# Kernel tuning notes

Hardware: AMD Instinct MI355X
Metric: run time of the kernel (lower is better)

Reference implementation:

```python
import jax, jax.numpy as jnp
import numpy as np

INP = 64   # inplanes
PLN = 64   # planes
LOC = 64   # loc_planes
EPS = 1e-5


def _linear_init(key, fan_in, fan_out):
    # torch nn.Linear default: U(-1/sqrt(fan_in), 1/sqrt(fan_in)) for W and b
    kw, kb = jax.random.split(key)
    bound = 1.0 / np.sqrt(fan_in)
    W = jax.random.uniform(kw, (fan_in, fan_out), jnp.float32, -bound, bound)
    b = jax.random.uniform(kb, (fan_out,), jnp.float32, -bound, bound)
    return W, b


def setup_inputs() -> dict:
    key = jax.random.key(0)
    ks = jax.random.split(key, 8)
    B, N = 8, 4096
    img_fea = jax.random.normal(ks[0], (B, N, INP), jnp.float32)
    loc_fea = jax.random.normal(ks[1], (B, N, LOC), jnp.float32)
    W11, b11 = _linear_init(ks[2], INP + LOC, INP)
    W12, b12 = _linear_init(ks[3], INP, INP)
    W21, b21 = _linear_init(ks[4], INP + LOC, INP)
    W22, b22 = _linear_init(ks[5], INP, INP * PLN)
    W3, b3 = _linear_init(ks[6], PLN, PLN)
    ln_g = jnp.ones((PLN,), jnp.float32)
    ln_b = jnp.zeros((PLN,), jnp.float32)
    return {
        "img_fea": img_fea, "loc_fea": loc_fea,
        "W11": W11, "b11": b11, "W12": W12, "b12": b12,
        "W21": W21, "b21": b21, "W22": W22, "b22": b22,
        "ln_g": ln_g, "ln_b": ln_b, "W3": W3, "b3": b3,
    }


def reference(img_fea, loc_fea, W11, b11, W12, b12, W21, b21, W22, b22,
              ln_g, ln_b, W3, b3):
    B, N, C = img_fea.shape
    cat_fea = jnp.concatenate([img_fea, loc_fea], axis=2)  # [B,N,INP+LOC]
    # branch 1: per-token input vector
    w11 = jax.nn.relu(cat_fea @ W11 + b11)                 # [B,N,INP]
    w12 = w11 @ W12 + b12                                  # [B,N,INP]
    # branch 2: per-token weight matrix generation
    w21 = jax.nn.relu(cat_fea @ W21 + b21)                 # [B,N,INP]
    w22 = (w21 @ W22 + b22).reshape(B, N, INP, PLN)        # [B,N,INP,PLN]
    # batched tiny matvec: (1,INP) @ (INP,PLN) per token
    x = jnp.einsum('bni,bnio->bno', w12, w22)              # [B,N,PLN]
    # LayerNorm over last dim + ReLU
    mu = jnp.mean(x, axis=-1, keepdims=True)
    var = jnp.mean(jnp.square(x - mu), axis=-1, keepdims=True)
    x = (x - mu) * jax.lax.rsqrt(var + EPS) * ln_g + ln_b
    x = jax.nn.relu(x)
    # final linear (no activation)
    return x @ W3 + b3
```

## Files before the change

kernel.cpp:

```cpp
#include <hip/hip_runtime.h>
#include <cstdint>


typedef __bf16 bf16x4 __attribute__((ext_vector_type(4)));
typedef __bf16 bf16x8 __attribute__((ext_vector_type(8)));
typedef float  f32x4  __attribute__((ext_vector_type(4)));

#define MFMA16(A, B, C) __builtin_amdgcn_mfma_f32_16x16x32_bf16(A, B, C, 0, 0, 0)

#define OFF_BT22 0
#define OFF_W11  266240
#define OFF_W21  274432
#define OFF_W12  282624
#define OFF_W3   286720

__global__ __launch_bounds__(256) void prep_kernel(
    const float* __restrict__ W22, const float* __restrict__ b22,
    const float* __restrict__ W11, const float* __restrict__ W21,
    const float* __restrict__ W12, const float* __restrict__ W3,
    __bf16* __restrict__ ws)
{
    __shared__ __bf16 T[64][72];
    const int b = blockIdx.x, tid = threadIdx.x;
    const float* src; long base = 0;
    if (b < 64)       { src = W22 + b * 4096; }
    else if (b == 64) { src = b22; }
    else if (b < 67)  { src = W11 + (b - 65) * 4096; base = OFF_W11 + (b - 65) * 4096; }
    else if (b < 69)  { src = W21 + (b - 67) * 4096; base = OFF_W21 + (b - 67) * 4096; }
    else if (b == 69) { src = W12;                   base = OFF_W12; }
    else              { src = W3;                    base = OFF_W3; }
    #pragma unroll
    for (int it = 0; it < 4; ++it) {
        int u = it * 1024 + tid * 4;
        int r = u >> 6, c = u & 63;
        const float4 v = *(const float4*)(src + u);
        T[r][c] = (__bf16)v.x; T[r][c + 1] = (__bf16)v.y;
        T[r][c + 2] = (__bf16)v.z; T[r][c + 3] = (__bf16)v.w;
    }
    __syncthreads();
    #pragma unroll
    for (int it = 0; it < 2; ++it) {
        int item = it * 256 + tid;
        int q = item >> 6, o = item & 63;
        bf16x8 pk;
        #pragma unroll
        for (int kj = 0; kj < 8; ++kj) pk[kj] = T[q * 8 + kj][o];
        long dstE;
        if (b <= 64) {
            int k8 = (b == 64 ? 512 : b * 8) + q;
            dstE = OFF_BT22 + ((long)(o >> 4) * 520 + k8) * 128 + (o & 15) * 8;
        } else {
            dstE = base + q * 512 + o * 8;
        }
        *(bf16x8*)(ws + dstE) = pk;
    }
}

#define LOADCH(buf, c) do {                                          \
    buf##_0 = *(const bf16x8*)(Bw + ((c)*16 +  0) * 128);            \
    buf##_1 = *(const bf16x8*)(Bw + ((c)*16 +  4) * 128);            \
    buf##_2 = *(const bf16x8*)(Bw + ((c)*16 +  8) * 128);            \
    buf##_3 = *(const bf16x8*)(Bw + ((c)*16 + 12) * 128);            \
} while (0)

#define COMPUTE_J(b0, b1, j) do {                                    \
    f32x4 w4[2];                                                     \
    _Pragma("unroll")                                                \
    for (int mf = 0; mf < 2; ++mf) {                                 \
        bf16x4 wv4 = *(const bf16x4*)(w21T + (j)*36 + mf*16 + quad*4);\
        w4[mf] = __builtin_convertvector(wv4, f32x4);                \
    }                                                                \
    _Pragma("unroll")                                                \
    for (int mf = 0; mf < 2; ++mf) {                                 \
        f32x4 fz = {};                                               \
        f32x4 m = MFMA16(a12[mf][0], b0, fz);                        \
        m       = MFMA16(a12[mf][1], b1, m);                         \
        _Pragma("unroll")                                            \
        for (int r = 0; r < 4; ++r)                                  \
            acc[mf][r] = fmaf(w4[mf][r], m[r], acc[mf][r]);          \
    }                                                                \
} while (0)

#define COMPUTE(buf, c) do {                                         \
    COMPUTE_J(buf##_0, buf##_1, (c)*2);                              \
    COMPUTE_J(buf##_2, buf##_3, (c)*2 + 1);                          \
} while (0)

__global__ __launch_bounds__(256, 4) void main_kernel(
    const float* __restrict__ img, const float* __restrict__ loc,
    const float* __restrict__ b11, const float* __restrict__ b12,
    const float* __restrict__ b21, const float* __restrict__ ln_g,
    const float* __restrict__ ln_b, const float* __restrict__ b3,
    const __bf16* __restrict__ ws, float* __restrict__ out)
{
    __shared__ __align__(1024) char smem[23552];
    __bf16* catL = (__bf16*)smem;
    __bf16* w11L = (__bf16*)(smem + 8704);
    __bf16* w12L = (__bf16*)(smem + 13312);
    __bf16* w21T = (__bf16*)(smem + 17920);
    float2* ps   = (float2*)(smem + 22528);
    __bf16* xL   = w11L;

    const int tid  = threadIdx.x;
    const int wv   = tid >> 6;
    const int lane = tid & 63;
    const int ln   = lane & 15;
    const int quad = lane >> 4;
    const int ob   = wv * 16;
    const long tb  = (long)blockIdx.x * 32;

    const __bf16* Bt22  = ws + OFF_BT22;
    const __bf16* W11bt = ws + OFF_W11;
    const __bf16* W21bt = ws + OFF_W21;
    const __bf16* W12bt = ws + OFF_W12;
    const __bf16* W3bt  = ws + OFF_W3;

    {
        const float* srcs[2] = {img, loc};
        #pragma unroll
        for (int s = 0; s < 2; ++s) {
            const float* src = srcs[s] + tb * 64;
            #pragma unroll
            for (int it = 0; it < 2; ++it) {
                int u = (it * 256 + tid) * 4;
                int t = u >> 6, c = u & 63;
                const float4 v = *(const float4*)(src + u);
                bf16x4 pk = {(__bf16)v.x, (__bf16)v.y, (__bf16)v.z, (__bf16)v.w};
                *(bf16x4*)(catL + t * 136 + s * 64 + c) = pk;
            }
        }
    }
    __syncthreads();

    {
        const int isW21 = wv >> 1;
        const int cb0 = (wv & 1) * 32;
        const __bf16* Wbt = isW21 ? W21bt : W11bt;
        const float* bsel = isW21 ? b21 : b11;
        f32x4 a1[2][2] = {};
        #pragma unroll
        for (int kb = 0; kb < 4; ++kb) {
            bf16x8 af[2];
            #pragma unroll
            for (int mf = 0; mf < 2; ++mf)
                af[mf] = *(const bf16x8*)(catL + (mf*16 + ln)*136 + kb*32 + quad*8);
            #pragma unroll
            for (int nf = 0; nf < 2; ++nf) {
                bf16x8 bw = *(const bf16x8*)(Wbt + ((kb*4 + quad)*64 + cb0 + nf*16 + ln)*8);
                #pragma unroll
                for (int mf = 0; mf < 2; ++mf)
                    a1[mf][nf] = MFMA16(af[mf], bw, a1[mf][nf]);
            }
        }
        if (!isW21) {
            #pragma unroll
            for (int nf = 0; nf < 2; ++nf) {
                int o = cb0 + nf*16 + ln;
                float cb = bsel[o];
                #pragma unroll
                for (int mf = 0; mf < 2; ++mf)
                    #pragma unroll
                    for (int r = 0; r < 4; ++r) {
                        int t = mf*16 + quad*4 + r;
                        float v = a1[mf][nf][r] + cb; v = v > 0.f ? v : 0.f;
                        w11L[t*72 + o] = (__bf16)v;
                    }
            }
        } else {
            #pragma unroll
            for (int nf = 0; nf < 2; ++nf) {
                int o = cb0 + nf*16 + ln;
                float cb = bsel[o];
                #pragma unroll
                for (int mf = 0; mf < 2; ++mf) {
                    bf16x4 pk;
                    #pragma unroll
                    for (int r = 0; r < 4; ++r) {
                        float v = a1[mf][nf][r] + cb; v = v > 0.f ? v : 0.f;
                        pk[r] = (__bf16)v;
                    }
                    *(bf16x4*)(w21T + o*36 + mf*16 + quad*4) = pk;
                }
            }
        }
    }
    __syncthreads();

    {
        float c12 = b12[ob + ln];
        f32x4 a12c[2] = {};
        #pragma unroll
        for (int kb = 0; kb < 2; ++kb) {
            bf16x8 bw = *(const bf16x8*)(W12bt + ((kb*4 + quad)*64 + ob + ln)*8);
            #pragma unroll
            for (int mf = 0; mf < 2; ++mf) {
                bf16x8 af = *(const bf16x8*)(w11L + (mf*16 + ln)*72 + kb*32 + quad*8);
                a12c[mf] = MFMA16(af, bw, a12c[mf]);
            }
        }
        #pragma unroll
        for (int mf = 0; mf < 2; ++mf)
            #pragma unroll
            for (int r = 0; r < 4; ++r) {
                int t = mf*16 + quad*4 + r;
                w12L[t*72 + ob + ln] = (__bf16)(a12c[mf][r] + c12);
            }
    }
    __syncthreads();

    bf16x8 a12[2][2];
    #pragma unroll
    for (int mf = 0; mf < 2; ++mf)
        #pragma unroll
        for (int sub = 0; sub < 2; ++sub)
            a12[mf][sub] = *(const bf16x8*)(w12L + (mf*16 + ln)*72 + sub*32 + quad*8);

    const __bf16* Bw = Bt22 + ((long)wv * 520 + quad) * 128 + ln * 8;

    bf16x8 B0_0, B0_1, B0_2, B0_3;
    bf16x8 B1_0, B1_1, B1_2, B1_3;

    f32x4 acc[2] = {};
    LOADCH(B0, 0);
    #pragma unroll 1
    for (int cc = 0; cc < 32; cc += 2) {
        LOADCH(B1, cc + 1);
        COMPUTE(B0, cc);
        if (cc + 2 < 32) LOADCH(B0, cc + 2);
        COMPUTE(B1, cc + 1);
    }
    {
        bf16x8 bb0 = *(const bf16x8*)(Bw + (512 + 0) * 128);
        bf16x8 bb1 = *(const bf16x8*)(Bw + (512 + 4) * 128);
        #pragma unroll
        for (int mf = 0; mf < 2; ++mf) {
            acc[mf] = MFMA16(a12[mf][0], bb0, acc[mf]);
            acc[mf] = MFMA16(a12[mf][1], bb1, acc[mf]);
        }
    }

    #pragma unroll
    for (int mf = 0; mf < 2; ++mf)
        #pragma unroll
        for (int r = 0; r < 4; ++r) {
            float v = acc[mf][r];
            float s1 = v, s2 = v*v;
            #pragma unroll
            for (int d = 1; d < 16; d <<= 1) {
                s1 += __shfl_xor(s1, d, 64);
                s2 += __shfl_xor(s2, d, 64);
            }
            if (ln == 0) {
                int t = mf*16 + quad*4 + r;
                ps[t*4 + wv] = make_float2(s1, s2);
            }
        }
    __syncthreads();

    float gv = ln_g[ob + ln], bv = ln_b[ob + ln], b3v = b3[ob + ln];
    #pragma unroll
    for (int mf = 0; mf < 2; ++mf)
        #pragma unroll
        for (int r = 0; r < 4; ++r) {
            int t = mf*16 + quad*4 + r;
            float2 p0 = ps[t*4], p1 = ps[t*4 + 1], p2 = ps[t*4 + 2], p3 = ps[t*4 + 3];
            float mean = (p0.x + p1.x + p2.x + p3.x) * 0.015625f;
            float var  = (p0.y + p1.y + p2.y + p3.y) * 0.015625f - mean * mean;
            float inv  = rsqrtf(var + 1e-5f);
            float v = (acc[mf][r] - mean) * inv * gv + bv;
            v = v > 0.f ? v : 0.f;
            xL[t*72 + ob + ln] = (__bf16)v;
        }
    __syncthreads();

    f32x4 a3[2] = {};
    #pragma unroll
    for (int kb = 0; kb < 2; ++kb) {
        bf16x8 bfr = *(const bf16x8*)(W3bt + ((kb*4 + quad)*64 + ob + ln)*8);
        #pragma unroll
        for (int mf = 0; mf < 2; ++mf) {
            bf16x8 af = *(const bf16x8*)(xL + (mf*16 + ln)*72 + kb*32 + quad*8);
            a3[mf] = MFMA16(af, bfr, a3[mf]);
        }
    }
    #pragma unroll
    for (int mf = 0; mf < 2; ++mf)
        #pragma unroll
        for (int r = 0; r < 4; ++r) {
            long t = tb + mf*16 + quad*4 + r;
            out[t*64 + ob + ln] = a3[mf][r] + b3v;
        }
}

extern "C" void kernel_launch(void* const* d_in, const int* in_sizes, int n_in,
                              void* d_out, int out_size, void* d_ws, size_t ws_size,
                              hipStream_t stream)
{
    const float* img  = (const float*)d_in[0];
    const float* loc  = (const float*)d_in[1];
    const float* W11  = (const float*)d_in[2];
    const float* b11  = (const float*)d_in[3];
    const float* W12  = (const float*)d_in[4];
    const float* b12  = (const float*)d_in[5];
    const float* W21  = (const float*)d_in[6];
    const float* b21  = (const float*)d_in[7];
    const float* W22  = (const float*)d_in[8];
    const float* b22  = (const float*)d_in[9];
    const float* ln_g = (const float*)d_in[10];
    const float* ln_b = (const float*)d_in[11];
    const float* W3   = (const float*)d_in[12];
    const float* b3   = (const float*)d_in[13];
    __bf16* ws = (__bf16*)d_ws;
    float*  o  = (float*)d_out;

    prep_kernel<<<71, 256, 0, stream>>>(W22, b22, W11, W21, W12, W3, ws);
    main_kernel<<<1024, 256, 0, stream>>>(img, loc, b11, b12, b21, ln_g, ln_b, b3, ws, o);
}
```

Measured before the change: 114.6 us.

## Fuse weight prep and main kernel via cooperative launch with grid sync

Merges the weight-repacking prep kernel into the main kernel. The first 71 blocks repack weights to bf16 while every block stages its input tile into shared memory, and a grid-wide sync separates the two phases. This removes one kernel launch and lets the input loads overlap the prep work. In exchange it needs a cooperative launch with all 1024 blocks co-resident and adds a grid barrier. If the cooperative launch fails, it falls back to the original two-kernel path.

```diff
diff --git a/kernel.cpp b/kernel.cpp
--- a/kernel.cpp
+++ b/kernel.cpp
@@ -1,5 +1,8 @@
 #include <hip/hip_runtime.h>
+#include <hip/hip_cooperative_groups.h>
 #include <cstdint>
+
+namespace cg = cooperative_groups;
 
 
 typedef __bf16 bf16x4 __attribute__((ext_vector_type(4)));
@@ -13,48 +16,6 @@
 #define OFF_W21  274432
 #define OFF_W12  282624
 #define OFF_W3   286720
-
-__global__ __launch_bounds__(256) void prep_kernel(
-    const float* __restrict__ W22, const float* __restrict__ b22,
-    const float* __restrict__ W11, const float* __restrict__ W21,
-    const float* __restrict__ W12, const float* __restrict__ W3,
-    __bf16* __restrict__ ws)
-{
-    __shared__ __bf16 T[64][72];
-    const int b = blockIdx.x, tid = threadIdx.x;
-    const float* src; long base = 0;
-    if (b < 64)       { src = W22 + b * 4096; }
-    else if (b == 64) { src = b22; }
-    else if (b < 67)  { src = W11 + (b - 65) * 4096; base = OFF_W11 + (b - 65) * 4096; }
-    else if (b < 69)  { src = W21 + (b - 67) * 4096; base = OFF_W21 + (b - 67) * 4096; }
-    else if (b == 69) { src = W12;                   base = OFF_W12; }
-    else              { src = W3;                    base = OFF_W3; }
-    #pragma unroll
-    for (int it = 0; it < 4; ++it) {
-        int u = it * 1024 + tid * 4;
-        int r = u >> 6, c = u & 63;
-        const float4 v = *(const float4*)(src + u);
-        T[r][c] = (__bf16)v.x; T[r][c + 1] = (__bf16)v.y;
-        T[r][c + 2] = (__bf16)v.z; T[r][c + 3] = (__bf16)v.w;
-    }
-    __syncthreads();
-    #pragma unroll
-    for (int it = 0; it < 2; ++it) {
-        int item = it * 256 + tid;
-        int q = item >> 6, o = item & 63;
-        bf16x8 pk;
-        #pragma unroll
-        for (int kj = 0; kj < 8; ++kj) pk[kj] = T[q * 8 + kj][o];
-        long dstE;
-        if (b <= 64) {
-            int k8 = (b == 64 ? 512 : b * 8) + q;
-            dstE = OFF_BT22 + ((long)(o >> 4) * 520 + k8) * 128 + (o & 15) * 8;
-        } else {
-            dstE = base + q * 512 + o * 8;
-        }
-        *(bf16x8*)(ws + dstE) = pk;
-    }
-}
 
 #define LOADCH(buf, c) do {                                          \
     buf##_0 = *(const bf16x8*)(Bw + ((c)*16 +  0) * 128);            \
@@ -85,6 +46,296 @@
     COMPUTE_J(buf##_0, buf##_1, (c)*2);                              \
     COMPUTE_J(buf##_2, buf##_3, (c)*2 + 1);                          \
 } while (0)
+
+__global__ __launch_bounds__(256, 4) void fused_kernel(
+    const float* __restrict__ img, const float* __restrict__ loc,
+    const float* __restrict__ b11, const float* __restrict__ b12,
+    const float* __restrict__ b21, const float* __restrict__ ln_g,
+    const float* __restrict__ ln_b, const float* __restrict__ b3,
+    const float* __restrict__ W22, const float* __restrict__ b22,
+    const float* __restrict__ W11, const float* __restrict__ W21,
+    const float* __restrict__ W12, const float* __restrict__ W3,
+    __bf16* __restrict__ ws, float* __restrict__ out)
+{
+    __shared__ __align__(1024) char smem[23552];
+    __bf16* catL = (__bf16*)smem;
+    __bf16* w11L = (__bf16*)(smem + 8704);
+    __bf16* w12L = (__bf16*)(smem + 13312);
+    __bf16* w21T = (__bf16*)(smem + 17920);
+    float2* ps   = (float2*)(smem + 22528);
+    __bf16* xL   = w11L;
+
+    const int tid  = threadIdx.x;
+    const int wv   = tid >> 6;
+    const int lane = tid & 63;
+    const int ln   = lane & 15;
+    const int quad = lane >> 4;
+    const int ob   = wv * 16;
+    const long tb  = (long)blockIdx.x * 32;
+
+    const __bf16* Bt22  = ws + OFF_BT22;
+    const __bf16* W11bt = ws + OFF_W11;
+    const __bf16* W21bt = ws + OFF_W21;
+    const __bf16* W12bt = ws + OFF_W12;
+    const __bf16* W3bt  = ws + OFF_W3;
+
+    {
+        const float* srcs[2] = {img, loc};
+        #pragma unroll
+        for (int s = 0; s < 2; ++s) {
+            const float* src = srcs[s] + tb * 64;
+            #pragma unroll
+            for (int it = 0; it < 2; ++it) {
+                int u = (it * 256 + tid) * 4;
+                int t = u >> 6, c = u & 63;
+                const float4 v = *(const float4*)(src + u);
+                bf16x4 pk = {(__bf16)v.x, (__bf16)v.y, (__bf16)v.z, (__bf16)v.w};
+                *(bf16x4*)(catL + t * 136 + s * 64 + c) = pk;
+            }
+        }
+    }
+
+    if (blockIdx.x < 71) {
+        __bf16 (*T)[72] = (__bf16 (*)[72])(smem + 8704);
+        const int b = blockIdx.x;
+        const float* src; long base = 0;
+        if (b < 64)       { src = W22 + b * 4096; }
+        else if (b == 64) { src = b22; }
+        else if (b < 67)  { src = W11 + (b - 65) * 4096; base = OFF_W11 + (b - 65) * 4096; }
+        else if (b < 69)  { src = W21 + (b - 67) * 4096; base = OFF_W21 + (b - 67) * 4096; }
+        else if (b == 69) { src = W12;                   base = OFF_W12; }
+        else              { src = W3;                    base = OFF_W3; }
+        #pragma unroll
+        for (int it = 0; it < 4; ++it) {
+            int u = it * 1024 + tid * 4;
+            int r = u >> 6, c = u & 63;
+            const float4 v = *(const float4*)(src + u);
+            T[r][c] = (__bf16)v.x; T[r][c + 1] = (__bf16)v.y;
+            T[r][c + 2] = (__bf16)v.z; T[r][c + 3] = (__bf16)v.w;
+        }
+        __syncthreads();
+        #pragma unroll
+        for (int it = 0; it < 2; ++it) {
+            int item = it * 256 + tid;
+            int q = item >> 6, o = item & 63;
+            bf16x8 pk;
+            #pragma unroll
+            for (int kj = 0; kj < 8; ++kj) pk[kj] = T[q * 8 + kj][o];
+            long dstE;
+            if (b <= 64) {
+                int k8 = (b == 64 ? 512 : b * 8) + q;
+                dstE = OFF_BT22 + ((long)(o >> 4) * 520 + k8) * 128 + (o & 15) * 8;
+            } else {
+                dstE = base + q * 512 + o * 8;
+            }
+            *(bf16x8*)(ws + dstE) = pk;
+        }
+    }
+
+    __threadfence();
+    cg::this_grid().sync();
+
+    {
+        const int isW21 = wv >> 1;
+        const int cb0 = (wv & 1) * 32;
+        const __bf16* Wbt = isW21 ? W21bt : W11bt;
+        const float* bsel = isW21 ? b21 : b11;
+        f32x4 a1[2][2] = {};
+        #pragma unroll
+        for (int kb = 0; kb < 4; ++kb) {
+            bf16x8 af[2];
+            #pragma unroll
+            for (int mf = 0; mf < 2; ++mf)
+                af[mf] = *(const bf16x8*)(catL + (mf*16 + ln)*136 + kb*32 + quad*8);
+            #pragma unroll
+            for (int nf = 0; nf < 2; ++nf) {
+                bf16x8 bw = *(const bf16x8*)(Wbt + ((kb*4 + quad)*64 + cb0 + nf*16 + ln)*8);
+                #pragma unroll
+                for (int mf = 0; mf < 2; ++mf)
+                    a1[mf][nf] = MFMA16(af[mf], bw, a1[mf][nf]);
+            }
+        }
+        if (!isW21) {
+            #pragma unroll
+            for (int nf = 0; nf < 2; ++nf) {
+                int o = cb0 + nf*16 + ln;
+                float cb = bsel[o];
+                #pragma unroll
+                for (int mf = 0; mf < 2; ++mf)
+                    #pragma unroll
+                    for (int r = 0; r < 4; ++r) {
+                        int t = mf*16 + quad*4 + r;
+                        float v = a1[mf][nf][r] + cb; v = v > 0.f ? v : 0.f;
+                        w11L[t*72 + o] = (__bf16)v;
+                    }
+            }
+        } else {
+            #pragma unroll
+            for (int nf = 0; nf < 2; ++nf) {
+                int o = cb0 + nf*16 + ln;
+                float cb = bsel[o];
+                #pragma unroll
+                for (int mf = 0; mf < 2; ++mf) {
+                    bf16x4 pk;
+                    #pragma unroll
+                    for (int r = 0; r < 4; ++r) {
+                        float v = a1[mf][nf][r] + cb; v = v > 0.f ? v : 0.f;
+                        pk[r] = (__bf16)v;
+                    }
+                    *(bf16x4*)(w21T + o*36 + mf*16 + quad*4) = pk;
+                }
+            }
+        }
+    }
+    __syncthreads();
+
+    {
+        float c12 = b12[ob + ln];
+        f32x4 a12c[2] = {};
+        #pragma unroll
+        for (int kb = 0; kb < 2; ++kb) {
+            bf16x8 bw = *(const bf16x8*)(W12bt + ((kb*4 + quad)*64 + ob + ln)*8);
+            #pragma unroll
+            for (int mf = 0; mf < 2; ++mf) {
+                bf16x8 af = *(const bf16x8*)(w11L + (mf*16 + ln)*72 + kb*32 + quad*8);
+                a12c[mf] = MFMA16(af, bw, a12c[mf]);
+            }
+        }
+        #pragma unroll
+        for (int mf = 0; mf < 2; ++mf)
+            #pragma unroll
+            for (int r = 0; r < 4; ++r) {
+                int t = mf*16 + quad*4 + r;
+                w12L[t*72 + ob + ln] = (__bf16)(a12c[mf][r] + c12);
+            }
+    }
+    __syncthreads();
+
+    bf16x8 a12[2][2];
+    #pragma unroll
+    for (int mf = 0; mf < 2; ++mf)
+        #pragma unroll
+        for (int sub = 0; sub < 2; ++sub)
+            a12[mf][sub] = *(const bf16x8*)(w12L + (mf*16 + ln)*72 + sub*32 + quad*8);
+
+    const __bf16* Bw = Bt22 + ((long)wv * 520 + quad) * 128 + ln * 8;
+
+    bf16x8 B0_0, B0_1, B0_2, B0_3;
+    bf16x8 B1_0, B1_1, B1_2, B1_3;
+
+    f32x4 acc[2] = {};
+    LOADCH(B0, 0);
+    #pragma unroll 1
+    for (int cc = 0; cc < 32; cc += 2) {
+        LOADCH(B1, cc + 1);
+        COMPUTE(B0, cc);
+        if (cc + 2 < 32) LOADCH(B0, cc + 2);
+        COMPUTE(B1, cc + 1);
+    }
+    {
+        bf16x8 bb0 = *(const bf16x8*)(Bw + (512 + 0) * 128);
+        bf16x8 bb1 = *(const bf16x8*)(Bw + (512 + 4) * 128);
+        #pragma unroll
+        for (int mf = 0; mf < 2; ++mf) {
+            acc[mf] = MFMA16(a12[mf][0], bb0, acc[mf]);
+            acc[mf] = MFMA16(a12[mf][1], bb1, acc[mf]);
+        }
+    }
+
+    #pragma unroll
+    for (int mf = 0; mf < 2; ++mf)
+        #pragma unroll
+        for (int r = 0; r < 4; ++r) {
+            float v = acc[mf][r];
+            float s1 = v, s2 = v*v;
+            #pragma unroll
+            for (int d = 1; d < 16; d <<= 1) {
+                s1 += __shfl_xor(s1, d, 64);
+                s2 += __shfl_xor(s2, d, 64);
+            }
+            if (ln == 0) {
+                int t = mf*16 + quad*4 + r;
+                ps[t*4 + wv] = make_float2(s1, s2);
+            }
+        }
+    __syncthreads();
+
+    float gv = ln_g[ob + ln], bv = ln_b[ob + ln], b3v = b3[ob + ln];
+    #pragma unroll
+    for (int mf = 0; mf < 2; ++mf)
+        #pragma unroll
+        for (int r = 0; r < 4; ++r) {
+            int t = mf*16 + quad*4 + r;
+            float2 p0 = ps[t*4], p1 = ps[t*4 + 1], p2 = ps[t*4 + 2], p3 = ps[t*4 + 3];
+            float mean = (p0.x + p1.x + p2.x + p3.x) * 0.015625f;
+            float var  = (p0.y + p1.y + p2.y + p3.y) * 0.015625f - mean * mean;
+            float inv  = rsqrtf(var + 1e-5f);
+            float v = (acc[mf][r] - mean) * inv * gv + bv;
+            v = v > 0.f ? v : 0.f;
+            xL[t*72 + ob + ln] = (__bf16)v;
+        }
+    __syncthreads();
+
+    f32x4 a3[2] = {};
+    #pragma unroll
+    for (int kb = 0; kb < 2; ++kb) {
+        bf16x8 bfr = *(const bf16x8*)(W3bt + ((kb*4 + quad)*64 + ob + ln)*8);
+        #pragma unroll
+        for (int mf = 0; mf < 2; ++mf) {
+            bf16x8 af = *(const bf16x8*)(xL + (mf*16 + ln)*72 + kb*32 + quad*8);
+            a3[mf] = MFMA16(af, bfr, a3[mf]);
+        }
+    }
+    #pragma unroll
+    for (int mf = 0; mf < 2; ++mf)
+        #pragma unroll
+        for (int r = 0; r < 4; ++r) {
+            long t = tb + mf*16 + quad*4 + r;
+            out[t*64 + ob + ln] = a3[mf][r] + b3v;
+        }
+}
+
+__global__ __launch_bounds__(256) void prep_kernel(
+    const float* __restrict__ W22, const float* __restrict__ b22,
+    const float* __restrict__ W11, const float* __restrict__ W21,
+    const float* __restrict__ W12, const float* __restrict__ W3,
+    __bf16* __restrict__ ws)
+{
+    __shared__ __bf16 T[64][72];
+    const int b = blockIdx.x, tid = threadIdx.x;
+    const float* src; long base = 0;
+    if (b < 64)       { src = W22 + b * 4096; }
+    else if (b == 64) { src = b22; }
+    else if (b < 67)  { src = W11 + (b - 65) * 4096; base = OFF_W11 + (b - 65) * 4096; }
+    else if (b < 69)  { src = W21 + (b - 67) * 4096; base = OFF_W21 + (b - 67) * 4096; }
+    else if (b == 69) { src = W12;                   base = OFF_W12; }
+    else              { src = W3;                    base = OFF_W3; }
+    #pragma unroll
+    for (int it = 0; it < 4; ++it) {
+        int u = it * 1024 + tid * 4;
+        int r = u >> 6, c = u & 63;
+        const float4 v = *(const float4*)(src + u);
+        T[r][c] = (__bf16)v.x; T[r][c + 1] = (__bf16)v.y;
+        T[r][c + 2] = (__bf16)v.z; T[r][c + 3] = (__bf16)v.w;
+    }
+    __syncthreads();
+    #pragma unroll
+    for (int it = 0; it < 2; ++it) {
+        int item = it * 256 + tid;
+        int q = item >> 6, o = item & 63;
+        bf16x8 pk;
+        #pragma unroll
+        for (int kj = 0; kj < 8; ++kj) pk[kj] = T[q * 8 + kj][o];
+        long dstE;
+        if (b <= 64) {
+            int k8 = (b == 64 ? 512 : b * 8) + q;
+            dstE = OFF_BT22 + ((long)(o >> 4) * 520 + k8) * 128 + (o & 15) * 8;
+        } else {
+            dstE = base + q * 512 + o * 8;
+        }
+        *(bf16x8*)(ws + dstE) = pk;
+    }
+}
 
 __global__ __launch_bounds__(256, 4) void main_kernel(
     const float* __restrict__ img, const float* __restrict__ loc,
@@ -313,6 +564,18 @@
     __bf16* ws = (__bf16*)d_ws;
     float*  o  = (float*)d_out;
 
-    prep_kernel<<<71, 256, 0, stream>>>(W22, b22, W11, W21, W12, W3, ws);
-    main_kernel<<<1024, 256, 0, stream>>>(img, loc, b11, b12, b21, ln_g, ln_b, b3, ws, o);
+    void* args[] = {
+        (void*)&img, (void*)&loc, (void*)&b11, (void*)&b12, (void*)&b21,
+        (void*)&ln_g, (void*)&ln_b, (void*)&b3, (void*)&W22, (void*)&b22,
+        (void*)&W11, (void*)&W21, (void*)&W12, (void*)&W3,
+        (void*)&ws, (void*)&o
+    };
+    hipError_t err = hipLaunchCooperativeKernel(
+        reinterpret_cast<void*>(fused_kernel), dim3(1024), dim3(256),
+        args, 0, stream);
+    if (err != hipSuccess) {
+        prep_kernel<<<71, 256, 0, stream>>>(W22, b22, W11, W21, W12, W3, ws);
+        main_kernel<<<1024, 256, 0, stream>>>(img, loc, b11, b12, b21,
+                                              ln_g, ln_b, b3, ws, o);
+    }
 }
```

Result: slower. 320.0 us (+179.3%).

## Double token tile per block and split W22 K-dimension across wave halves

Applied to the files above, without the earlier changes.

Each block now handles 64 tokens with 512 threads (8 waves). The waves split the generated-weight reduction over the input dimension into two halves, and partial accumulators are combined through shared memory before LayerNorm. Each streamed W22 chunk is now reused across twice as many tokens, which halves global/L2 weight traffic per token. The cost is doubled LDS use, extra synchronisation and a combine step, and only half the waves do the LayerNorm work.

```diff
diff --git a/kernel.cpp b/kernel.cpp
--- a/kernel.cpp
+++ b/kernel.cpp
@@ -64,14 +64,14 @@
 } while (0)
 
 #define COMPUTE_J(b0, b1, j) do {                                    \
-    f32x4 w4[2];                                                     \
+    f32x4 w4[4];                                                     \
     _Pragma("unroll")                                                \
-    for (int mf = 0; mf < 2; ++mf) {                                 \
-        bf16x4 wv4 = *(const bf16x4*)(w21T + (j)*36 + mf*16 + quad*4);\
+    for (int mf = 0; mf < 4; ++mf) {                                 \
+        bf16x4 wv4 = *(const bf16x4*)(w21Tk + (j)*72 + mf*16 + quad*4);\
         w4[mf] = __builtin_convertvector(wv4, f32x4);                \
     }                                                                \
     _Pragma("unroll")                                                \
-    for (int mf = 0; mf < 2; ++mf) {                                 \
+    for (int mf = 0; mf < 4; ++mf) {                                 \
         f32x4 fz = {};                                               \
         f32x4 m = MFMA16(a12[mf][0], b0, fz);                        \
         m       = MFMA16(a12[mf][1], b1, m);                         \
@@ -86,28 +86,31 @@
     COMPUTE_J(buf##_2, buf##_3, (c)*2 + 1);                          \
 } while (0)
 
-__global__ __launch_bounds__(256, 4) void main_kernel(
+__global__ __launch_bounds__(512, 4) void main_kernel(
     const float* __restrict__ img, const float* __restrict__ loc,
     const float* __restrict__ b11, const float* __restrict__ b12,
     const float* __restrict__ b21, const float* __restrict__ ln_g,
     const float* __restrict__ ln_b, const float* __restrict__ b3,
     const __bf16* __restrict__ ws, float* __restrict__ out)
 {
-    __shared__ __align__(1024) char smem[23552];
+    __shared__ __align__(1024) char smem[47104];
     __bf16* catL = (__bf16*)smem;
-    __bf16* w11L = (__bf16*)(smem + 8704);
-    __bf16* w12L = (__bf16*)(smem + 13312);
-    __bf16* w21T = (__bf16*)(smem + 17920);
-    float2* ps   = (float2*)(smem + 22528);
+    __bf16* w11L = (__bf16*)(smem + 17408);
+    __bf16* w12L = (__bf16*)(smem + 26624);
+    __bf16* w21T = (__bf16*)(smem + 35840);
+    float2* ps   = (float2*)(smem + 45056);
+    float*  combL = (float*)smem;
     __bf16* xL   = w11L;
 
     const int tid  = threadIdx.x;
     const int wv   = tid >> 6;
+    const int og   = wv & 3;
+    const int kh   = wv >> 2;
     const int lane = tid & 63;
     const int ln   = lane & 15;
     const int quad = lane >> 4;
-    const int ob   = wv * 16;
-    const long tb  = (long)blockIdx.x * 32;
+    const int ob   = og * 16;
+    const long tb  = (long)blockIdx.x * 64;
 
     const __bf16* Bt22  = ws + OFF_BT22;
     const __bf16* W11bt = ws + OFF_W11;
@@ -122,7 +125,7 @@
             const float* src = srcs[s] + tb * 64;
             #pragma unroll
             for (int it = 0; it < 2; ++it) {
-                int u = (it * 256 + tid) * 4;
+                int u = (it * 512 + tid) * 4;
                 int t = u >> 6, c = u & 63;
                 const float4 v = *(const float4*)(src + u);
                 bf16x4 pk = {(__bf16)v.x, (__bf16)v.y, (__bf16)v.z, (__bf16)v.w};
@@ -133,54 +136,39 @@
     __syncthreads();
 
     {
-        const int isW21 = wv >> 1;
-        const int cb0 = (wv & 1) * 32;
+        const int isW21 = kh;
         const __bf16* Wbt = isW21 ? W21bt : W11bt;
         const float* bsel = isW21 ? b21 : b11;
-        f32x4 a1[2][2] = {};
+        f32x4 a1[4] = {};
         #pragma unroll
         for (int kb = 0; kb < 4; ++kb) {
-            bf16x8 af[2];
-            #pragma unroll
-            for (int mf = 0; mf < 2; ++mf)
-                af[mf] = *(const bf16x8*)(catL + (mf*16 + ln)*136 + kb*32 + quad*8);
-            #pragma unroll
-            for (int nf = 0; nf < 2; ++nf) {
-                bf16x8 bw = *(const bf16x8*)(Wbt + ((kb*4 + quad)*64 + cb0 + nf*16 + ln)*8);
+            bf16x8 bw = *(const bf16x8*)(Wbt + ((kb*4 + quad)*64 + ob + ln)*8);
+            #pragma unroll
+            for (int mf = 0; mf < 4; ++mf) {
+                bf16x8 af = *(const bf16x8*)(catL + (mf*16 + ln)*136 + kb*32 + quad*8);
+                a1[mf] = MFMA16(af, bw, a1[mf]);
+            }
+        }
+        float cb = bsel[ob + ln];
+        if (!isW21) {
+            #pragma unroll
+            for (int mf = 0; mf < 4; ++mf)
                 #pragma unroll
-                for (int mf = 0; mf < 2; ++mf)
-                    a1[mf][nf] = MFMA16(af[mf], bw, a1[mf][nf]);
-            }
-        }
-        if (!isW21) {
-            #pragma unroll
-            for (int nf = 0; nf < 2; ++nf) {
-                int o = cb0 + nf*16 + ln;
-                float cb = bsel[o];
+                for (int r = 0; r < 4; ++r) {
+                    int t = mf*16 + quad*4 + r;
+                    float v = a1[mf][r] + cb; v = v > 0.f ? v : 0.f;
+                    w11L[t*72 + ob + ln] = (__bf16)v;
+                }
+        } else {
+            #pragma unroll
+            for (int mf = 0; mf < 4; ++mf) {
+                bf16x4 pk;
                 #pragma unroll
-                for (int mf = 0; mf < 2; ++mf)
-                    #pragma unroll
-                    for (int r = 0; r < 4; ++r) {
-                        int t = mf*16 + quad*4 + r;
-                        float v = a1[mf][nf][r] + cb; v = v > 0.f ? v : 0.f;
-                        w11L[t*72 + o] = (__bf16)v;
-                    }
-            }
-        } else {
-            #pragma unroll
-            for (int nf = 0; nf < 2; ++nf) {
-                int o = cb0 + nf*16 + ln;
-                float cb = bsel[o];
-                #pragma unroll
-                for (int mf = 0; mf < 2; ++mf) {
-                    bf16x4 pk;
-                    #pragma unroll
-                    for (int r = 0; r < 4; ++r) {
-                        float v = a1[mf][nf][r] + cb; v = v > 0.f ? v : 0.f;
-                        pk[r] = (__bf16)v;
-                    }
-                    *(bf16x4*)(w21T + o*36 + mf*16 + quad*4) = pk;
+                for (int r = 0; r < 4; ++r) {
+                    float v = a1[mf][r] + cb; v = v > 0.f ? v : 0.f;
+                    pk[r] = (__bf16)v;
                 }
+                *(bf16x4*)(w21T + (ob + ln)*72 + mf*16 + quad*4) = pk;
             }
         }
     }
@@ -194,7 +182,7 @@
             bf16x8 bw = *(const bf16x8*)(W12bt + ((kb*4 + quad)*64 + ob + ln)*8);
             #pragma unroll
             for (int mf = 0; mf < 2; ++mf) {
-                bf16x8 af = *(const bf16x8*)(w11L + (mf*16 + ln)*72 + kb*32 + quad*8);
+                bf16x8 af = *(const bf16x8*)(w11L + (kh*32 + mf*16 + ln)*72 + kb*32 + quad*8);
                 a12c[mf] = MFMA16(af, bw, a12c[mf]);
             }
         }
@@ -202,94 +190,113 @@
         for (int mf = 0; mf < 2; ++mf)
             #pragma unroll
             for (int r = 0; r < 4; ++r) {
-                int t = mf*16 + quad*4 + r;
+                int t = kh*32 + mf*16 + quad*4 + r;
                 w12L[t*72 + ob + ln] = (__bf16)(a12c[mf][r] + c12);
             }
     }
     __syncthreads();
 
-    bf16x8 a12[2][2];
+    bf16x8 a12[4][2];
     #pragma unroll
-    for (int mf = 0; mf < 2; ++mf)
+    for (int mf = 0; mf < 4; ++mf)
         #pragma unroll
         for (int sub = 0; sub < 2; ++sub)
             a12[mf][sub] = *(const bf16x8*)(w12L + (mf*16 + ln)*72 + sub*32 + quad*8);
 
-    const __bf16* Bw = Bt22 + ((long)wv * 520 + quad) * 128 + ln * 8;
+    const __bf16* BwBase = Bt22 + ((long)og * 520 + quad) * 128 + ln * 8;
+    const __bf16* Bw     = BwBase + (long)kh * 32768;
+    const __bf16* w21Tk  = w21T + kh * 32 * 72;
 
     bf16x8 B0_0, B0_1, B0_2, B0_3;
     bf16x8 B1_0, B1_1, B1_2, B1_3;
 
-    f32x4 acc[2] = {};
+    f32x4 acc[4] = {};
     LOADCH(B0, 0);
     #pragma unroll 1
-    for (int cc = 0; cc < 32; cc += 2) {
+    for (int cc = 0; cc < 16; cc += 2) {
         LOADCH(B1, cc + 1);
         COMPUTE(B0, cc);
-        if (cc + 2 < 32) LOADCH(B0, cc + 2);
+        if (cc + 2 < 16) LOADCH(B0, cc + 2);
         COMPUTE(B1, cc + 1);
     }
-    {
-        bf16x8 bb0 = *(const bf16x8*)(Bw + (512 + 0) * 128);
-        bf16x8 bb1 = *(const bf16x8*)(Bw + (512 + 4) * 128);
-        #pragma unroll
-        for (int mf = 0; mf < 2; ++mf) {
+    if (kh == 1) {
+        bf16x8 bb0 = *(const bf16x8*)(BwBase + (512 + 0) * 128);
+        bf16x8 bb1 = *(const bf16x8*)(BwBase + (512 + 4) * 128);
+        #pragma unroll
+        for (int mf = 0; mf < 4; ++mf) {
             acc[mf] = MFMA16(a12[mf][0], bb0, acc[mf]);
             acc[mf] = MFMA16(a12[mf][1], bb1, acc[mf]);
         }
     }
 
-    #pragma unroll
-    for (int mf = 0; mf < 2; ++mf)
-        #pragma unroll
-        for (int r = 0; r < 4; ++r) {
-            float v = acc[mf][r];
-            float s1 = v, s2 = v*v;
-            #pragma unroll
-            for (int d = 1; d < 16; d <<= 1) {
-                s1 += __shfl_xor(s1, d, 64);
-                s2 += __shfl_xor(s2, d, 64);
-            }
-            if (ln == 0) {
+    if (kh == 1) {
+        #pragma unroll
+        for (int mf = 0; mf < 4; ++mf)
+            #pragma unroll
+            for (int r = 0; r < 4; ++r) {
                 int t = mf*16 + quad*4 + r;
-                ps[t*4 + wv] = make_float2(s1, s2);
-            }
-        }
-    __syncthreads();
-
-    float gv = ln_g[ob + ln], bv = ln_b[ob + ln], b3v = b3[ob + ln];
-    #pragma unroll
-    for (int mf = 0; mf < 2; ++mf)
-        #pragma unroll
-        for (int r = 0; r < 4; ++r) {
-            int t = mf*16 + quad*4 + r;
-            float2 p0 = ps[t*4], p1 = ps[t*4 + 1], p2 = ps[t*4 + 2], p3 = ps[t*4 + 3];
-            float mean = (p0.x + p1.x + p2.x + p3.x) * 0.015625f;
-            float var  = (p0.y + p1.y + p2.y + p3.y) * 0.015625f - mean * mean;
-            float inv  = rsqrtf(var + 1e-5f);
-            float v = (acc[mf][r] - mean) * inv * gv + bv;
-            v = v > 0.f ? v : 0.f;
-            xL[t*72 + ob + ln] = (__bf16)v;
-        }
-    __syncthreads();
-
-    f32x4 a3[2] = {};
-    #pragma unroll
-    for (int kb = 0; kb < 2; ++kb) {
-        bf16x8 bfr = *(const bf16x8*)(W3bt + ((kb*4 + quad)*64 + ob + ln)*8);
-        #pragma unroll
-        for (int mf = 0; mf < 2; ++mf) {
-            bf16x8 af = *(const bf16x8*)(xL + (mf*16 + ln)*72 + kb*32 + quad*8);
-            a3[mf] = MFMA16(af, bfr, a3[mf]);
-        }
-    }
-    #pragma unroll
-    for (int mf = 0; mf < 2; ++mf)
-        #pragma unroll
-        for (int r = 0; r < 4; ++r) {
-            long t = tb + mf*16 + quad*4 + r;
-            out[t*64 + ob + ln] = a3[mf][r] + b3v;
-        }
+                combL[og*1088 + t*17 + ln] = acc[mf][r];
+            }
+    }
+    __syncthreads();
+
+    if (kh == 0) {
+        #pragma unroll
+        for (int mf = 0; mf < 4; ++mf)
+            #pragma unroll
+            for (int r = 0; r < 4; ++r) {
+                int t = mf*16 + quad*4 + r;
+                acc[mf][r] += combL[og*1088 + t*17 + ln];
+                float v = acc[mf][r];
+                float s1 = v, s2 = v*v;
+                #pragma unroll
+                for (int d = 1; d < 16; d <<= 1) {
+                    s1 += __shfl_xor(s1, d, 64);
+                    s2 += __shfl_xor(s2, d, 64);
+                }
+                if (ln == 0) ps[t*4 + og] = make_float2(s1, s2);
+            }
+    }
+    __syncthreads();
+
+    if (kh == 0) {
+        float gv = ln_g[ob + ln], bv = ln_b[ob + ln];
+        #pragma unroll
+        for (int mf = 0; mf < 4; ++mf)
+            #pragma unroll
+            for (int r = 0; r < 4; ++r) {
+                int t = mf*16 + quad*4 + r;
+                float2 p0 = ps[t*4], p1 = ps[t*4 + 1], p2 = ps[t*4 + 2], p3 = ps[t*4 + 3];
+                float mean = (p0.x + p1.x + p2.x + p3.x) * 0.015625f;
+                float var  = (p0.y + p1.y + p2.y + p3.y) * 0.015625f - mean * mean;
+                float inv  = rsqrtf(var + 1e-5f);
+                float v = (acc[mf][r] - mean) * inv * gv + bv;
+                v = v > 0.f ? v : 0.f;
+                xL[t*72 + ob + ln] = (__bf16)v;
+            }
+    }
+    __syncthreads();
+
+    {
+        float b3v = b3[ob + ln];
+        f32x4 a3[2] = {};
+        #pragma unroll
+        for (int kb = 0; kb < 2; ++kb) {
+            bf16x8 bfr = *(const bf16x8*)(W3bt + ((kb*4 + quad)*64 + ob + ln)*8);
+            #pragma unroll
+            for (int mf = 0; mf < 2; ++mf) {
+                bf16x8 af = *(const bf16x8*)(xL + (kh*32 + mf*16 + ln)*72 + kb*32 + quad*8);
+                a3[mf] = MFMA16(af, bfr, a3[mf]);
+            }
+        }
+        #pragma unroll
+        for (int mf = 0; mf < 2; ++mf)
+            #pragma unroll
+            for (int r = 0; r < 4; ++r) {
+                long t = tb + kh*32 + mf*16 + quad*4 + r;
+                out[t*64 + ob + ln] = a3[mf][r] + b3v;
+            }
+    }
 }
 
 extern "C" void kernel_launch(void* const* d_in, const int* in_sizes, int n_in,
@@ -314,5 +321,5 @@
     float*  o  = (float*)d_out;
 
     prep_kernel<<<71, 256, 0, stream>>>(W22, b22, W11, W21, W12, W3, ws);
-    main_kernel<<<1024, 256, 0, stream>>>(img, loc, b11, b12, b21, ln_g, ln_b, b3, ws, o);
+    main_kernel<<<512, 512, 0, stream>>>(img, loc, b11, b12, b21, ln_g, ln_b, b3, ws, o);
 }
```

Measured after the change: 184.7 us. 1.61x slower.
